# Kernel optimization log

Measured on AMD Instinct MI355X. Metric: run time of the kernel, lower is better.

Reference implementation:

```python
import jax, jax.numpy as jnp
import numpy as np

NUM_HEADS = 16
NUM_KV_HEADS = 4
HEAD_DIM = 128
ROPE_THETA = 10000.0
LN_EPS = 1e-5


def rotate_half(x):
    h = x.shape[-1] // 2
    return jnp.concatenate([-x[..., h:], x[..., :h]], axis=-1)


def setup_inputs() -> dict:
    key = jax.random.key(0)
    ks = jax.random.split(key, 12)
    B, S, H = 2, 2048, 2048
    qdim = NUM_HEADS * HEAD_DIM          # 2048
    kvdim = NUM_KV_HEADS * HEAD_DIM      # 512
    s = 1.0 / np.sqrt(H)
    return {
        'hidden_states': jax.random.normal(ks[0], (B, S, H), jnp.float32),
        'position_ids': jnp.arange(S, dtype=jnp.int32).reshape(1, S),
        'Wq': jax.random.normal(ks[1], (H, qdim), jnp.float32) * s,
        'Wk': jax.random.normal(ks[2], (H, kvdim), jnp.float32) * s,
        'Wv': jax.random.normal(ks[3], (H, kvdim), jnp.float32) * s,
        'Wo': jax.random.normal(ks[4], (qdim, H), jnp.float32) * (1.0 / np.sqrt(qdim)),
        'Wg1': jax.random.normal(ks[5], (H, NUM_HEADS), jnp.float32) * s,
        'bg1': jnp.zeros((NUM_HEADS,), jnp.float32),
        'Wg2': jax.random.normal(ks[6], (H, NUM_HEADS), jnp.float32) * s,
        'bg2': jnp.zeros((NUM_HEADS,), jnp.float32),
        'ln_gamma': jnp.ones((HEAD_DIM,), jnp.float32),
        'ln_beta': jnp.zeros((HEAD_DIM,), jnp.float32),
    }


def reference(hidden_states, position_ids, Wq, Wk, Wv, Wo, Wg1, bg1, Wg2, bg2, ln_gamma, ln_beta):
    B, S, H = hidden_states.shape
    dt = hidden_states.dtype

    # q/k/v projections -> (B, heads, S, head_dim)
    q = (hidden_states @ Wq).reshape(B, S, NUM_HEADS, HEAD_DIM).transpose(0, 2, 1, 3)
    k = (hidden_states @ Wk).reshape(B, S, NUM_KV_HEADS, HEAD_DIM).transpose(0, 2, 1, 3)
    v = (hidden_states @ Wv).reshape(B, S, NUM_KV_HEADS, HEAD_DIM).transpose(0, 2, 1, 3)

    # Llama RoPE
    inv_freq = 1.0 / (ROPE_THETA ** (jnp.arange(0, HEAD_DIM, 2, dtype=jnp.float32) / HEAD_DIM))
    freqs = position_ids.astype(jnp.float32)[..., None] * inv_freq  # (1, S, hd/2)
    emb = jnp.concatenate([freqs, freqs], axis=-1)                  # (1, S, hd)
    cos = jnp.cos(emb)[:, None].astype(dt)                          # (1, 1, S, hd)
    sin = jnp.sin(emb)[:, None].astype(dt)
    q = q * cos + rotate_half(q) * sin
    k = k * cos + rotate_half(k) * sin

    # GQA: repeat kv heads
    n_rep = NUM_HEADS // NUM_KV_HEADS
    k = jnp.repeat(k, n_rep, axis=1)
    v = jnp.repeat(v, n_rep, axis=1)

    # per-token per-head gates: (B, S, heads) -> (B, heads, S, 1)
    g1 = jax.nn.sigmoid(hidden_states @ Wg1 + bg1).transpose(0, 2, 1)[..., None]
    g2 = jax.nn.sigmoid(hidden_states @ Wg2 + bg2).transpose(0, 2, 1)[..., None]

    # value gating (weight_proj2)
    v = v * g2

    # causal softmax attention
    scores = jnp.einsum('bhqd,bhkd->bhqk', q, k) / np.sqrt(HEAD_DIM)
    causal = jnp.tril(jnp.ones((S, S), bool))
    scores = jnp.where(causal[None, None], scores, jnp.finfo(jnp.float32).min)
    probs = jax.nn.softmax(scores.astype(jnp.float32), axis=-1).astype(dt)
    o = jnp.einsum('bhqk,bhkd->bhqd', probs, v)  # (B, heads, S, hd)

    # per-head LayerNorm over head_dim, then output gating (weight_proj)
    mu = jnp.mean(o, axis=-1, keepdims=True)
    var = jnp.mean(jnp.square(o - mu), axis=-1, keepdims=True)
    o = (o - mu) / jnp.sqrt(var + LN_EPS) * ln_gamma + ln_beta
    o = o * g1

    o = o.transpose(0, 2, 1, 3).reshape(B, S, NUM_HEADS * HEAD_DIM)
    return o @ Wo
```

## Files before the change

### kernel.cpp

```cpp
#include <hip/hip_runtime.h>
#include <hip/hip_bf16.h>
#include <stdint.h>
#include <string.h>

using bf16 = __hip_bfloat16;
typedef __attribute__((ext_vector_type(8))) short bf16x8;
typedef __attribute__((ext_vector_type(4))) float f32x4;

#define DEV static __device__ __forceinline__

DEV bf16 tobf(float f) { return __float2bfloat16(f); }
DEV float tof(bf16 h) { return __bfloat162float(h); }

DEV void gload_lds16(const void* g, void* l) {
  __builtin_amdgcn_global_load_lds((__attribute__((address_space(1))) void*)g,
                                   (__attribute__((address_space(3))) void*)l,
                                   16, 0, 0);
}


__global__ void transpose_cast_k(const float* __restrict__ src, bf16* __restrict__ dst,
                                 int K, int N) {
  __shared__ float tile[32][33];
  int kb = blockIdx.x * 32, nb = blockIdx.y * 32;
  int tx = threadIdx.x, ty = threadIdx.y;
#pragma unroll
  for (int i = 0; i < 32; i += 8)
    tile[ty + i][tx] = src[(size_t)(kb + ty + i) * N + nb + tx];
  __syncthreads();
#pragma unroll
  for (int i = 0; i < 32; i += 8)
    dst[(size_t)(nb + ty + i) * K + kb + tx] = tobf(tile[tx][ty + i]);
}

__global__ void gw_transpose_k(const float* __restrict__ Wg1, const float* __restrict__ Wg2,
                               bf16* __restrict__ dstbase) {
  int g = blockIdx.x >> 4, r = blockIdx.x & 15;
  const float* src = g ? Wg2 : Wg1;
  bf16* dst = dstbase + (size_t)(3072 + g * 16 + r) * 2048;
  for (int k = threadIdx.x; k < 2048; k += 256) dst[k] = tobf(src[(size_t)k * 16 + r]);
}

__global__ void cast_x_k(const float* __restrict__ src, bf16* __restrict__ dst) {
  int i = blockIdx.x * blockDim.x + threadIdx.x;
  float4 v = ((const float4*)src)[i];
  bf16 t[4] = {tobf(v.x), tobf(v.y), tobf(v.z), tobf(v.w)};
  uint2 p; __builtin_memcpy(&p, t, 8);
  ((uint2*)dst)[i] = p;
}

__global__ void rope_table_k(const int* __restrict__ pos, float* __restrict__ cosT,
                             float* __restrict__ sinT) {
  int s = blockIdx.x, i = threadIdx.x;
  double inv = exp(-((double)(2 * i) / 128.0) * log(10000.0));
  float f = (float)pos[s] * (float)inv;
  cosT[s * 64 + i] = cosf(f);
  sinT[s * 64 + i] = sinf(f);
}

__global__ __launch_bounds__(256) void rope_apply_k(
    bf16* __restrict__ qkv, const float* __restrict__ cosT, const float* __restrict__ sinT) {
  int idx = blockIdx.x * 256 + threadIdx.x;
  int c = idx & 7, hh = idx >> 3;
  int head = hh % 20, t = hh / 20;
  int s = t & 2047;
  size_t base = (size_t)t * 3072 + (head < 16 ? head * 128 : 2048 + (head - 16) * 128);
  int d0 = c * 8;
  bf16x8 lo = *(const bf16x8*)(qkv + base + d0);
  bf16x8 hi = *(const bf16x8*)(qkv + base + d0 + 64);
  float4 c0 = *(const float4*)(cosT + s * 64 + d0);
  float4 c1 = *(const float4*)(cosT + s * 64 + d0 + 4);
  float4 s0 = *(const float4*)(sinT + s * 64 + d0);
  float4 s1 = *(const float4*)(sinT + s * 64 + d0 + 4);
  float cs[8] = {c0.x, c0.y, c0.z, c0.w, c1.x, c1.y, c1.z, c1.w};
  float sn[8] = {s0.x, s0.y, s0.z, s0.w, s1.x, s1.y, s1.z, s1.w};
  bf16x8 olo, ohi;
#pragma unroll
  for (int j = 0; j < 8; j++) {
    float a = tof(((const bf16*)&lo)[j]), b = tof(((const bf16*)&hi)[j]);
    ((bf16*)&olo)[j] = tobf(a * cs[j] - b * sn[j]);
    ((bf16*)&ohi)[j] = tobf(b * cs[j] + a * sn[j]);
  }
  *(bf16x8*)(qkv + base + d0) = olo;
  *(bf16x8*)(qkv + base + d0 + 64) = ohi;
}

__global__ __launch_bounds__(256, 2) void gemm_qkv_k(
    const bf16* __restrict__ A, const bf16* __restrict__ Bt, bf16* __restrict__ qkv,
    float* __restrict__ g1t, float* __restrict__ g2t,
    const float* __restrict__ bg1, const float* __restrict__ bg2) {
  constexpr int BK = 32, K = 2048;
  __shared__ bf16 sA[2][128 * BK];
  __shared__ bf16 sB[2][128 * BK];
  const int tid = threadIdx.x, wave = tid >> 6, lane = tid & 63;
  const int lhi = lane >> 4, llo = lane & 15;
  const int wm = wave >> 1, wn = wave & 1;
  const int bm = blockIdx.y, bn = blockIdx.x;
  const bf16* Ag = A + (size_t)bm * 128 * K;
  const bf16* Bg = Bt + (size_t)bn * 128 * K;

  f32x4 acc[4][4];
#pragma unroll
  for (int m = 0; m < 4; m++)
#pragma unroll
    for (int n = 0; n < 4; n++) acc[m][n] = f32x4{0.f, 0.f, 0.f, 0.f};

  auto stage = [&](int buf, int kt) {
#pragma unroll
    for (int i = 0; i < 2; i++) {
      int c = i * 256 + tid, row = c >> 2, c8 = c & 3;
      gload_lds16(Ag + (size_t)row * K + kt * BK + c8 * 8, &sA[buf][c * 8]);
    }
#pragma unroll
    for (int i = 0; i < 2; i++) {
      int c = i * 256 + tid, row = c >> 2, c8 = c & 3;
      gload_lds16(Bg + (size_t)row * K + kt * BK + c8 * 8, &sB[buf][c * 8]);
    }
  };

  const int NT = K / BK;
  stage(0, 0);
  for (int kt = 0; kt < NT; kt++) {
    __syncthreads();
    if (kt + 1 < NT) stage((kt + 1) & 1, kt + 1);
    const bf16* a_ = sA[kt & 1];
    const bf16* b_ = sB[kt & 1];
    bf16x8 af[4], bfr[4];
#pragma unroll
    for (int m = 0; m < 4; m++)
      af[m] = *(const bf16x8*)&a_[(wm * 64 + m * 16 + llo) * BK + lhi * 8];
#pragma unroll
    for (int n = 0; n < 4; n++)
      bfr[n] = *(const bf16x8*)&b_[(wn * 64 + n * 16 + llo) * BK + lhi * 8];
#pragma unroll
    for (int m = 0; m < 4; m++)
#pragma unroll
      for (int n = 0; n < 4; n++)
        acc[m][n] = __builtin_amdgcn_mfma_f32_16x16x32_bf16(af[m], bfr[n], acc[m][n], 0, 0, 0);
  }

  const int r0 = bm * 128 + wm * 64, c0 = bn * 128 + wn * 64;
#pragma unroll
  for (int m = 0; m < 4; m++)
#pragma unroll
    for (int n = 0; n < 4; n++) {
      int col = c0 + n * 16 + llo;
#pragma unroll
      for (int r = 0; r < 4; r++) {
        int row = r0 + m * 16 + lhi * 4 + r;
        if (col < 3072) {
          qkv[(size_t)row * 3072 + col] = tobf(acc[m][n][r]);
        } else if (col < 3104) {
          int idx = col - 3072, hh = idx & 15;
          float b = (idx < 16) ? bg1[hh] : bg2[hh];
          float v = 1.f / (1.f + __expf(-(acc[m][n][r] + b)));
          ((idx < 16) ? g1t : g2t)[(size_t)hh * 4096 + row] = v;
        }
      }
    }
}

__global__ __launch_bounds__(256, 2) void gemm_out_k(
    const bf16* __restrict__ A, const bf16* __restrict__ Bt, float* __restrict__ C,
    int M, int N, int K) {
  constexpr int BK = 32;
  __shared__ bf16 sA[2][128 * BK];
  __shared__ bf16 sB[2][128 * BK];
  const int tid = threadIdx.x, wave = tid >> 6, lane = tid & 63;
  const int lhi = lane >> 4, llo = lane & 15;
  const int wm = wave >> 1, wn = wave & 1;
  const int bm = blockIdx.y, bn = blockIdx.x;
  const bf16* Ag = A + (size_t)bm * 128 * K;
  const bf16* Bg = Bt + (size_t)bn * 128 * K;

  f32x4 acc[4][4];
#pragma unroll
  for (int m = 0; m < 4; m++)
#pragma unroll
    for (int n = 0; n < 4; n++) acc[m][n] = f32x4{0.f, 0.f, 0.f, 0.f};

  auto stage = [&](int buf, int kt) {
#pragma unroll
    for (int i = 0; i < 2; i++) {
      int c = i * 256 + tid, row = c >> 2, c8 = c & 3;
      gload_lds16(Ag + (size_t)row * K + kt * BK + c8 * 8, &sA[buf][c * 8]);
    }
#pragma unroll
    for (int i = 0; i < 2; i++) {
      int c = i * 256 + tid, row = c >> 2, c8 = c & 3;
      gload_lds16(Bg + (size_t)row * K + kt * BK + c8 * 8, &sB[buf][c * 8]);
    }
  };

  const int NT = K / BK;
  stage(0, 0);
  for (int kt = 0; kt < NT; kt++) {
    __syncthreads();
    if (kt + 1 < NT) stage((kt + 1) & 1, kt + 1);
    const bf16* a_ = sA[kt & 1];
    const bf16* b_ = sB[kt & 1];
    bf16x8 af[4], bfr[4];
#pragma unroll
    for (int m = 0; m < 4; m++)
      af[m] = *(const bf16x8*)&a_[(wm * 64 + m * 16 + llo) * BK + lhi * 8];
#pragma unroll
    for (int n = 0; n < 4; n++)
      bfr[n] = *(const bf16x8*)&b_[(wn * 64 + n * 16 + llo) * BK + lhi * 8];
#pragma unroll
    for (int m = 0; m < 4; m++)
#pragma unroll
      for (int n = 0; n < 4; n++)
        acc[m][n] = __builtin_amdgcn_mfma_f32_16x16x32_bf16(af[m], bfr[n], acc[m][n], 0, 0, 0);
  }

  const int r0 = bm * 128 + wm * 64, c0 = bn * 128 + wn * 64;
#pragma unroll
  for (int m = 0; m < 4; m++)
#pragma unroll
    for (int n = 0; n < 4; n++)
#pragma unroll
      for (int r = 0; r < 4; r++)
        C[(size_t)(r0 + m * 16 + lhi * 4 + r) * N + (c0 + n * 16 + llo)] = acc[m][n][r];
}

DEV void finalize_store(const f32x4 (&o)[8], int wave, int lhi, int llo, int tid,
                        int h, int qt, size_t tok0,
                        const float* __restrict__ g1t, const float* __restrict__ lng,
                        const float* __restrict__ lnb, bf16* sK, bf16* __restrict__ aout) {
  float sum[4] = {0, 0, 0, 0}, sq[4] = {0, 0, 0, 0};
#pragma unroll
  for (int dt = 0; dt < 8; dt++)
#pragma unroll
    for (int r = 0; r < 4; r++) {
      float v = o[dt][r];
      sum[r] += v;
      sq[r] += v * v;
    }
  float mu[4], rstd[4];
#pragma unroll
  for (int r = 0; r < 4; r++) {
    float s1 = sum[r], s2 = sq[r];
    s1 += __shfl_xor(s1, 1); s1 += __shfl_xor(s1, 2); s1 += __shfl_xor(s1, 4); s1 += __shfl_xor(s1, 8);
    s2 += __shfl_xor(s2, 1); s2 += __shfl_xor(s2, 2); s2 += __shfl_xor(s2, 4); s2 += __shfl_xor(s2, 8);
    float m_ = s1 * (1.f / 128.f);
    float var = s2 * (1.f / 128.f) - m_ * m_;
    mu[r] = m_;
    rstd[r] = rsqrtf(var + 1e-5f);
  }
  __syncthreads();
#pragma unroll
  for (int r = 0; r < 4; r++) {
    int lrow = wave * 16 + lhi * 4 + r;
    float gg = g1t[(size_t)h * 4096 + tok0 + qt * 64 + lrow];
#pragma unroll
    for (int dt = 0; dt < 8; dt++) {
      int d = dt * 16 + llo;
      float v = (o[dt][r] - mu[r]) * rstd[r] * lng[d] + lnb[d];
      sK[lrow * 128 + d] = tobf(v * gg);
    }
  }
  __syncthreads();
#pragma unroll
  for (int i = 0; i < 4; i++) {
    int c = i * 256 + tid, lr = c >> 4, c8 = c & 15;
    *(uint4*)(aout + (tok0 + qt * 64 + lr) * 2048 + h * 128 + c8 * 8) =
        *(const uint4*)&sK[lr * 128 + c8 * 8];
  }
}

__global__ __launch_bounds__(256, 2) void attn_split_k(
    const bf16* __restrict__ qkv, const float* __restrict__ g2t,
    const float* __restrict__ g1t, const float* __restrict__ lng,
    const float* __restrict__ lnb,
    float* __restrict__ pO, float* __restrict__ pML, bf16* __restrict__ aout) {
  constexpr int S = 2048, LD = 3072;
  const int bid = blockIdx.x;
  const int g = bid & 7, j = bid >> 3;
  const int hp = j & 1, u = j >> 1;
  int qt, k0, s;
  bool partial;
  if (u < 16) { qt = 16 + u; k0 = 0; s = 0; partial = true; }
  else {
    int p = (u - 16) >> 1;
    if (((u - 16) & 1) == 0) { qt = 15 - p; k0 = 0; s = 0; partial = false; }
    else { qt = 31 - p; k0 = 16; s = 1; partial = true; }
  }
  const int k1 = (u < 16) ? 16 : qt + 1;

  const int b = g >> 2, kvh = g & 3, h0 = kvh * 4 + hp * 2;
  const int tid = threadIdx.x, wave = tid >> 6, lane = tid & 63;
  const int lhi = lane >> 4, llo = lane & 15;
  const size_t tok0 = (size_t)b * S;

  __shared__ bf16 sK[64 * 128];
  __shared__ bf16 sV[128 * 64];
  __shared__ bf16 sP[4][2][16][72];

  const int qrow0 = qt * 64 + wave * 16;

  bf16x8 qf[2][4];
#pragma unroll
  for (int hh = 0; hh < 2; hh++) {
    const bf16* qg = qkv + (tok0 + qrow0 + llo) * LD + (h0 + hh) * 128;
#pragma unroll
    for (int dc = 0; dc < 4; dc++) qf[hh][dc] = *(const bf16x8*)(qg + dc * 32 + lhi * 8);
  }

  f32x4 oacc[2][8];
#pragma unroll
  for (int hh = 0; hh < 2; hh++)
#pragma unroll
    for (int i = 0; i < 8; i++) oacc[hh][i] = f32x4{0.f, 0.f, 0.f, 0.f};
  float mrow[2][4], lrow[2][4];
#pragma unroll
  for (int hh = 0; hh < 2; hh++)
#pragma unroll
    for (int r = 0; r < 4; r++) { mrow[hh][r] = -1e30f; lrow[hh][r] = 0.f; }
  const float scale = 0.08838834764831845f;

  uint4 kreg[4];
  bf16x8 vreg[4];
  float gvreg[2];
  const int vdg = tid >> 4;
  const int vkg = tid & 15;

  auto issue_loads = [&](int kt) {
#pragma unroll
    for (int i = 0; i < 4; i++) {
      int c = i * 256 + tid, row = c >> 4, c8 = c & 15;
      kreg[i] = *(const uint4*)(qkv + (tok0 + kt * 64 + row) * LD + 2048 + kvh * 128 + c8 * 8);
    }
#pragma unroll
    for (int r = 0; r < 4; r++)
      vreg[r] = *(const bf16x8*)(qkv + (tok0 + kt * 64 + vkg * 4 + r) * LD + 2560 +
                                 kvh * 128 + vdg * 8);
#pragma unroll
    for (int hh = 0; hh < 2; hh++)
      gvreg[hh] = g2t[(size_t)(h0 + hh) * 4096 + tok0 + kt * 64 + lane];
  };

  auto write_lds = [&]() {
#pragma unroll
    for (int i = 0; i < 4; i++) {
      int c = i * 256 + tid, row = c >> 4, c8 = c & 15;
      int eidx = (row * 128 + c8 * 8) ^ ((row & 7) << 3);
      *(uint4*)&sK[eidx] = kreg[i];
    }
#pragma unroll
    for (int e = 0; e < 8; e++) {
      int d = vdg * 8 + e;
      uint32_t lo = (uint32_t)(unsigned short)vreg[0][e] |
                    ((uint32_t)(unsigned short)vreg[1][e] << 16);
      uint32_t hi = (uint32_t)(unsigned short)vreg[2][e] |
                    ((uint32_t)(unsigned short)vreg[3][e] << 16);
      int eidx = (d * 64 + vkg * 4) ^ (e << 3);
      uint2 pk; pk.x = lo; pk.y = hi;
      *(uint2*)&sV[eidx] = pk;
    }
  };

  issue_loads(k0);
  for (int kt = k0; kt < k1; kt++) {
    __syncthreads();
    write_lds();
    float gv0 = gvreg[0], gv1 = gvreg[1];
    __syncthreads();
    if (kt + 1 < k1) issue_loads(kt + 1);

    const bool diag = (kt == qt);
#pragma unroll
    for (int hh = 0; hh < 2; hh++) {
      f32x4 sc[4];
#pragma unroll
      for (int ct = 0; ct < 4; ct++) {
        f32x4 acc = f32x4{0.f, 0.f, 0.f, 0.f};
#pragma unroll
        for (int dc = 0; dc < 4; dc++) {
          int row = ct * 16 + llo;
          bf16x8 kf = *(const bf16x8*)&sK[(row * 128 + dc * 32 + lhi * 8) ^ ((row & 7) << 3)];
          acc = __builtin_amdgcn_mfma_f32_16x16x32_bf16(qf[hh][dc], kf, acc, 0, 0, 0);
        }
        sc[ct] = acc;
      }
      float pm[4] = {-1e30f, -1e30f, -1e30f, -1e30f};
#pragma unroll
      for (int ct = 0; ct < 4; ct++) {
        int kv = kt * 64 + ct * 16 + llo;
#pragma unroll
        for (int r = 0; r < 4; r++) {
          float s_ = sc[ct][r] * scale;
          if (diag && kv > qrow0 + lhi * 4 + r) s_ = -1e30f;
          sc[ct][r] = s_;
          pm[r] = fmaxf(pm[r], s_);
        }
      }
#pragma unroll
      for (int r = 0; r < 4; r++) {
        float v = pm[r];
        v = fmaxf(v, __shfl_xor(v, 1));
        v = fmaxf(v, __shfl_xor(v, 2));
        v = fmaxf(v, __shfl_xor(v, 4));
        v = fmaxf(v, __shfl_xor(v, 8));
        pm[r] = v;
      }
      int need = 0;
#pragma unroll
      for (int r = 0; r < 4; r++) need |= (pm[r] > mrow[hh][r]) ? 1 : 0;
      if (__any(need)) {
#pragma unroll
        for (int r = 0; r < 4; r++) {
          float mnew = fmaxf(mrow[hh][r], pm[r]);
          float al = __expf(mrow[hh][r] - mnew);
          mrow[hh][r] = mnew;
          lrow[hh][r] *= al;
#pragma unroll
          for (int i = 0; i < 8; i++) oacc[hh][i][r] *= al;
        }
      }
      float gv = hh ? gv1 : gv0;
      float g2v[4];
#pragma unroll
      for (int ct = 0; ct < 4; ct++) g2v[ct] = __shfl(gv, ct * 16 + llo);
      float rs[4] = {0.f, 0.f, 0.f, 0.f};
#pragma unroll
      for (int ct = 0; ct < 4; ct++) {
#pragma unroll
        for (int r = 0; r < 4; r++) {
          float p = __expf(sc[ct][r] - mrow[hh][r]);
          rs[r] += p;
          sP[wave][hh][lhi * 4 + r][ct * 16 + llo] = tobf(p * g2v[ct]);
        }
      }
#pragma unroll
      for (int r = 0; r < 4; r++) {
        float v = rs[r];
        v += __shfl_xor(v, 1); v += __shfl_xor(v, 2); v += __shfl_xor(v, 4); v += __shfl_xor(v, 8);
        lrow[hh][r] += v;
      }
    }
#pragma unroll
    for (int kc = 0; kc < 2; kc++) {
      bf16x8 pf0 = *(const bf16x8*)&sP[wave][0][llo][kc * 32 + lhi * 8];
      bf16x8 pf1 = *(const bf16x8*)&sP[wave][1][llo][kc * 32 + lhi * 8];
#pragma unroll
      for (int dt = 0; dt < 8; dt++) {
        int d = dt * 16 + llo;
        bf16x8 vf = *(const bf16x8*)&sV[(d * 64 + kc * 32 + lhi * 8) ^ ((d & 7) << 3)];
        oacc[0][dt] = __builtin_amdgcn_mfma_f32_16x16x32_bf16(pf0, vf, oacc[0][dt], 0, 0, 0);
        oacc[1][dt] = __builtin_amdgcn_mfma_f32_16x16x32_bf16(pf1, vf, oacc[1][dt], 0, 0, 0);
      }
    }
  }

  if (partial) {
    const int combo = (qt - 16) * 2 + s;
#pragma unroll
    for (int hh = 0; hh < 2; hh++) {
      const int sub = (g * 2 + hp) * 2 + hh;
      f32x4* dst = (f32x4*)pO + (size_t)(combo * 32 + sub) * 2048;
#pragma unroll
      for (int dt = 0; dt < 8; dt++)
        dst[(wave * 8 + dt) * 64 + lane] = oacc[hh][dt];
      if (llo == 0) {
#pragma unroll
        for (int r = 0; r < 4; r++) {
          int row = wave * 16 + lhi * 4 + r;
          float* pm = pML + ((size_t)(combo * 32 + sub) * 64 + row) * 2;
          pm[0] = mrow[hh][r];
          pm[1] = lrow[hh][r];
        }
      }
    }
  } else {
#pragma unroll
    for (int hh = 0; hh < 2; hh++) {
      float inv[4];
#pragma unroll
      for (int r = 0; r < 4; r++) inv[r] = 1.f / lrow[hh][r];
      f32x4 o[8];
#pragma unroll
      for (int dt = 0; dt < 8; dt++)
#pragma unroll
        for (int r = 0; r < 4; r++) o[dt][r] = oacc[hh][dt][r] * inv[r];
      finalize_store(o, wave, lhi, llo, tid, h0 + hh, qt, tok0, g1t, lng, lnb, sK, aout);
    }
  }
}

__global__ __launch_bounds__(256) void attn_combine_k(
    const float* __restrict__ pO, const float* __restrict__ pML,
    const float* __restrict__ g1t, const float* __restrict__ lng,
    const float* __restrict__ lnb, bf16* __restrict__ aout) {
  __shared__ bf16 sK[64 * 128];
  const int bid = blockIdx.x;
  const int g = bid & 7, j = bid >> 3;
  const int hp = j & 1, qt16 = j >> 1;
  const int qt = 16 + qt16;
  const int b = g >> 2, kvh = g & 3, h0 = kvh * 4 + hp * 2;
  const int tid = threadIdx.x, wave = tid >> 6, lane = tid & 63;
  const int lhi = lane >> 4, llo = lane & 15;
  const size_t tok0 = (size_t)b * 2048;
  const int c0 = qt16 * 2, c1 = qt16 * 2 + 1;
#pragma unroll
  for (int hh = 0; hh < 2; hh++) {
    const int sub = (g * 2 + hp) * 2 + hh;
    const f32x4* p0 = (const f32x4*)pO + (size_t)(c0 * 32 + sub) * 2048;
    const f32x4* p1 = (const f32x4*)pO + (size_t)(c1 * 32 + sub) * 2048;
    float w0[4], w1[4], inv[4];
#pragma unroll
    for (int r = 0; r < 4; r++) {
      int row = wave * 16 + lhi * 4 + r;
      const float* q0 = pML + ((size_t)(c0 * 32 + sub) * 64 + row) * 2;
      const float* q1 = pML + ((size_t)(c1 * 32 + sub) * 64 + row) * 2;
      float m0 = q0[0], l0 = q0[1], m1 = q1[0], l1 = q1[1];
      float ms = fmaxf(m0, m1);
      w0[r] = __expf(m0 - ms);
      w1[r] = __expf(m1 - ms);
      inv[r] = 1.f / (w0[r] * l0 + w1[r] * l1);
    }
    f32x4 o[8];
#pragma unroll
    for (int dt = 0; dt < 8; dt++) {
      f32x4 a = p0[(wave * 8 + dt) * 64 + lane];
      f32x4 c = p1[(wave * 8 + dt) * 64 + lane];
#pragma unroll
      for (int r = 0; r < 4; r++) o[dt][r] = (w0[r] * a[r] + w1[r] * c[r]) * inv[r];
    }
    finalize_store(o, wave, lhi, llo, tid, h0 + hh, qt, tok0, g1t, lng, lnb, sK, aout);
  }
}

extern "C" void kernel_launch(void* const* d_in, const int* in_sizes, int n_in,
                              void* d_out, int out_size, void* d_ws, size_t ws_size,
                              hipStream_t stream) {
  (void)in_sizes; (void)n_in; (void)out_size; (void)ws_size;
  const float* X   = (const float*)d_in[0];
  const int*   pos = (const int*)d_in[1];
  const float* Wq  = (const float*)d_in[2];
  const float* Wk  = (const float*)d_in[3];
  const float* Wv  = (const float*)d_in[4];
  const float* Wo  = (const float*)d_in[5];
  const float* Wg1 = (const float*)d_in[6];
  const float* bg1 = (const float*)d_in[7];
  const float* Wg2 = (const float*)d_in[8];
  const float* bg2 = (const float*)d_in[9];
  const float* lng = (const float*)d_in[10];
  const float* lnb = (const float*)d_in[11];

  char* ws = (char*)d_ws;
  size_t off = 0;
  auto alloc = [&](size_t bytes) {
    void* p = ws + off;
    off += (bytes + 255) & ~(size_t)255;
    return p;
  };
  bf16*  WT   = (bf16*)alloc(3200ull * 2048 * 2);
  bf16*  WoT  = (bf16*)alloc(2048ull * 2048 * 2);
  bf16*  Xbf  = (bf16*)alloc(4096ull * 2048 * 2);
  bf16*  qkv  = (bf16*)alloc(4096ull * 3072 * 2);
  bf16*  attn = (bf16*)alloc(4096ull * 2048 * 2);
  float* cosT = (float*)alloc(2048ull * 64 * 4);
  float* sinT = (float*)alloc(2048ull * 64 * 4);
  float* g1t  = (float*)alloc(16ull * 4096 * 4);
  float* g2t  = (float*)alloc(16ull * 4096 * 4);
  float* pO   = (float*)alloc(32ull * 32 * 8192 * 4);
  float* pML  = (float*)alloc(32ull * 32 * 64 * 2 * 4);

  dim3 tb(32, 8);
  transpose_cast_k<<<dim3(64, 64), tb, 0, stream>>>(Wq, WT, 2048, 2048);
  transpose_cast_k<<<dim3(64, 16), tb, 0, stream>>>(Wk, WT + 2048ull * 2048, 2048, 512);
  transpose_cast_k<<<dim3(64, 16), tb, 0, stream>>>(Wv, WT + 2560ull * 2048, 2048, 512);
  transpose_cast_k<<<dim3(64, 64), tb, 0, stream>>>(Wo, WoT, 2048, 2048);
  gw_transpose_k<<<32, 256, 0, stream>>>(Wg1, Wg2, WT);
  cast_x_k<<<8192, 256, 0, stream>>>(X, Xbf);
  rope_table_k<<<2048, 64, 0, stream>>>(pos, cosT, sinT);

  gemm_qkv_k<<<dim3(25, 32), 256, 0, stream>>>(Xbf, WT, qkv, g1t, g2t, bg1, bg2);
  rope_apply_k<<<2560, 256, 0, stream>>>(qkv, cosT, sinT);
  attn_split_k<<<768, 256, 0, stream>>>(qkv, g2t, g1t, lng, lnb, pO, pML, attn);
  attn_combine_k<<<256, 256, 0, stream>>>(pO, pML, g1t, lng, lnb, attn);
  gemm_out_k<<<dim3(16, 32), 256, 0, stream>>>(attn, WoT, (float*)d_out, 4096, 2048, 2048);
}
```

Before: 296.4 us.

## Split causal attention into 8-tile KV chunks with table-driven scheduling

Replaces the two-way split of causal attention with chunks of at most 8 KV tiles, so query tiles beyond 8 are split into 2-4 partials. A lookup table orders the work units longest-first for load balancing, and the combine kernel now merges up to 4 partials. Launch bounds rise to 3 blocks per SM, and the next tile's loads are issued before the barrier. The aim is better balance and occupancy, at the cost of more partial-result traffic, more combine work and possible register pressure.

```diff
diff --git a/kernel.cpp b/kernel.cpp
--- a/kernel.cpp
+++ b/kernel.cpp
@@ -268,7 +268,28 @@
   }
 }
 
-__global__ __launch_bounds__(256, 2) void attn_split_k(
+DEV int pid_base(int qt) {
+  return qt < 8 ? qt : qt < 16 ? 2 * qt - 8 : qt < 24 ? 3 * qt - 24 : 4 * qt - 48;
+}
+
+__device__ const unsigned char UNIT_TAB[80] = {
+  124,125,126,127,
+  120,121,122, 116,117,118, 112,113,114,
+  108,109,110, 104,105,106, 100,101,102,
+   96, 97, 98,  92, 93, 94,
+   88, 89,  84, 85,  80, 81,  76, 77,
+   72, 73,  68, 69,  64, 65,  60, 61,
+   56, 52, 48, 44, 40, 36, 32, 28,
+  123, 90, 57, 24,
+  119, 86, 53, 20,
+  115, 82, 49, 16,
+  111, 78, 45, 12,
+  107, 74, 41,  8,
+  103, 70, 37,  4,
+   99, 66, 33,  0
+};
+
+__global__ __launch_bounds__(256, 3) void attn_split_k(
     const bf16* __restrict__ qkv, const float* __restrict__ g2t,
     const float* __restrict__ g1t, const float* __restrict__ lng,
     const float* __restrict__ lnb,
@@ -277,15 +298,10 @@
   const int bid = blockIdx.x;
   const int g = bid & 7, j = bid >> 3;
   const int hp = j & 1, u = j >> 1;
-  int qt, k0, s;
-  bool partial;
-  if (u < 16) { qt = 16 + u; k0 = 0; s = 0; partial = true; }
-  else {
-    int p = (u - 16) >> 1;
-    if (((u - 16) & 1) == 0) { qt = 15 - p; k0 = 0; s = 0; partial = false; }
-    else { qt = 31 - p; k0 = 16; s = 1; partial = true; }
-  }
-  const int k1 = (u < 16) ? 16 : qt + 1;
+  const int e = UNIT_TAB[u];
+  const int qt = e >> 2, s = e & 3;
+  const int k0 = s * 8, k1 = min(s * 8 + 8, qt + 1);
+  const bool partial = (qt >= 8);
 
   const int b = g >> 2, kvh = g & 3, h0 = kvh * 4 + hp * 2;
   const int tid = threadIdx.x, wave = tid >> 6, lane = tid & 63;
@@ -347,13 +363,13 @@
       *(uint4*)&sK[eidx] = kreg[i];
     }
 #pragma unroll
-    for (int e = 0; e < 8; e++) {
-      int d = vdg * 8 + e;
-      uint32_t lo = (uint32_t)(unsigned short)vreg[0][e] |
-                    ((uint32_t)(unsigned short)vreg[1][e] << 16);
-      uint32_t hi = (uint32_t)(unsigned short)vreg[2][e] |
-                    ((uint32_t)(unsigned short)vreg[3][e] << 16);
-      int eidx = (d * 64 + vkg * 4) ^ (e << 3);
+    for (int e2 = 0; e2 < 8; e2++) {
+      int d = vdg * 8 + e2;
+      uint32_t lo = (uint32_t)(unsigned short)vreg[0][e2] |
+                    ((uint32_t)(unsigned short)vreg[1][e2] << 16);
+      uint32_t hi = (uint32_t)(unsigned short)vreg[2][e2] |
+                    ((uint32_t)(unsigned short)vreg[3][e2] << 16);
+      int eidx = (d * 64 + vkg * 4) ^ (e2 << 3);
       uint2 pk; pk.x = lo; pk.y = hi;
       *(uint2*)&sV[eidx] = pk;
     }
@@ -364,8 +380,8 @@
     __syncthreads();
     write_lds();
     float gv0 = gvreg[0], gv1 = gvreg[1];
+    if (kt + 1 < k1) issue_loads(kt + 1);
     __syncthreads();
-    if (kt + 1 < k1) issue_loads(kt + 1);
 
     const bool diag = (kt == qt);
 #pragma unroll
@@ -453,11 +469,11 @@
   }
 
   if (partial) {
-    const int combo = (qt - 16) * 2 + s;
+    const int pid = pid_base(qt) + s;
 #pragma unroll
     for (int hh = 0; hh < 2; hh++) {
       const int sub = (g * 2 + hp) * 2 + hh;
-      f32x4* dst = (f32x4*)pO + (size_t)(combo * 32 + sub) * 2048;
+      f32x4* dst = (f32x4*)pO + (size_t)(pid * 32 + sub) * 2048;
 #pragma unroll
       for (int dt = 0; dt < 8; dt++)
         dst[(wave * 8 + dt) * 64 + lane] = oacc[hh][dt];
@@ -465,7 +481,7 @@
 #pragma unroll
         for (int r = 0; r < 4; r++) {
           int row = wave * 16 + lhi * 4 + r;
-          float* pm = pML + ((size_t)(combo * 32 + sub) * 64 + row) * 2;
+          float* pm = pML + ((size_t)(pid * 32 + sub) * 64 + row) * 2;
           pm[0] = mrow[hh][r];
           pm[1] = lrow[hh][r];
         }
@@ -494,37 +510,49 @@
   __shared__ bf16 sK[64 * 128];
   const int bid = blockIdx.x;
   const int g = bid & 7, j = bid >> 3;
-  const int hp = j & 1, qt16 = j >> 1;
-  const int qt = 16 + qt16;
+  const int hp = j & 1, qtc = j >> 1;
+  const int qt = 8 + qtc;
+  const int ns = (qt < 16) ? 2 : (qt < 24) ? 3 : 4;
+  const int p0id = pid_base(qt);
   const int b = g >> 2, kvh = g & 3, h0 = kvh * 4 + hp * 2;
   const int tid = threadIdx.x, wave = tid >> 6, lane = tid & 63;
   const int lhi = lane >> 4, llo = lane & 15;
   const size_t tok0 = (size_t)b * 2048;
-  const int c0 = qt16 * 2, c1 = qt16 * 2 + 1;
 #pragma unroll
   for (int hh = 0; hh < 2; hh++) {
     const int sub = (g * 2 + hp) * 2 + hh;
-    const f32x4* p0 = (const f32x4*)pO + (size_t)(c0 * 32 + sub) * 2048;
-    const f32x4* p1 = (const f32x4*)pO + (size_t)(c1 * 32 + sub) * 2048;
-    float w0[4], w1[4], inv[4];
+    float w[4][4], inv[4];
 #pragma unroll
     for (int r = 0; r < 4; r++) {
       int row = wave * 16 + lhi * 4 + r;
-      const float* q0 = pML + ((size_t)(c0 * 32 + sub) * 64 + row) * 2;
-      const float* q1 = pML + ((size_t)(c1 * 32 + sub) * 64 + row) * 2;
-      float m0 = q0[0], l0 = q0[1], m1 = q1[0], l1 = q1[1];
-      float ms = fmaxf(m0, m1);
-      w0[r] = __expf(m0 - ms);
-      w1[r] = __expf(m1 - ms);
-      inv[r] = 1.f / (w0[r] * l0 + w1[r] * l1);
+      float m[4], l[4], ms = -1e30f;
+#pragma unroll
+      for (int sp = 0; sp < 4; sp++)
+        if (sp < ns) {
+          const float* q = pML + ((size_t)((p0id + sp) * 32 + sub) * 64 + row) * 2;
+          m[sp] = q[0]; l[sp] = q[1];
+          ms = fmaxf(ms, m[sp]);
+        }
+      float L = 0.f;
+#pragma unroll
+      for (int sp = 0; sp < 4; sp++)
+        if (sp < ns) { w[sp][r] = __expf(m[sp] - ms); L += w[sp][r] * l[sp]; }
+      inv[r] = 1.f / L;
     }
     f32x4 o[8];
 #pragma unroll
     for (int dt = 0; dt < 8; dt++) {
-      f32x4 a = p0[(wave * 8 + dt) * 64 + lane];
-      f32x4 c = p1[(wave * 8 + dt) * 64 + lane];
-#pragma unroll
-      for (int r = 0; r < 4; r++) o[dt][r] = (w0[r] * a[r] + w1[r] * c[r]) * inv[r];
+      f32x4 a = f32x4{0.f, 0.f, 0.f, 0.f};
+#pragma unroll
+      for (int sp = 0; sp < 4; sp++)
+        if (sp < ns) {
+          f32x4 c = ((const f32x4*)pO + (size_t)((p0id + sp) * 32 + sub) * 2048)
+                        [(wave * 8 + dt) * 64 + lane];
+#pragma unroll
+          for (int r = 0; r < 4; r++) a[r] += w[sp][r] * c[r];
+        }
+#pragma unroll
+      for (int r = 0; r < 4; r++) o[dt][r] = a[r] * inv[r];
     }
     finalize_store(o, wave, lhi, llo, tid, h0 + hh, qt, tok0, g1t, lng, lnb, sK, aout);
   }
@@ -563,8 +591,8 @@
   float* sinT = (float*)alloc(2048ull * 64 * 4);
   float* g1t  = (float*)alloc(16ull * 4096 * 4);
   float* g2t  = (float*)alloc(16ull * 4096 * 4);
-  float* pO   = (float*)alloc(32ull * 32 * 8192 * 4);
-  float* pML  = (float*)alloc(32ull * 32 * 64 * 2 * 4);
+  float* pO   = (float*)alloc(80ull * 32 * 8192 * 4);
+  float* pML  = (float*)alloc(80ull * 32 * 64 * 2 * 4);
 
   dim3 tb(32, 8);
   transpose_cast_k<<<dim3(64, 64), tb, 0, stream>>>(Wq, WT, 2048, 2048);
@@ -577,7 +605,7 @@
 
   gemm_qkv_k<<<dim3(25, 32), 256, 0, stream>>>(Xbf, WT, qkv, g1t, g2t, bg1, bg2);
   rope_apply_k<<<2560, 256, 0, stream>>>(qkv, cosT, sinT);
-  attn_split_k<<<768, 256, 0, stream>>>(qkv, g2t, g1t, lng, lnb, pO, pML, attn);
-  attn_combine_k<<<256, 256, 0, stream>>>(pO, pML, g1t, lng, lnb, attn);
+  attn_split_k<<<1280, 256, 0, stream>>>(qkv, g2t, g1t, lng, lnb, pO, pML, attn);
+  attn_combine_k<<<384, 256, 0, stream>>>(pO, pML, g1t, lng, lnb, attn);
   gemm_out_k<<<dim3(16, 32), 256, 0, stream>>>(attn, WoT, (float*)d_out, 4096, 2048, 2048);
 }
```

Result: slower. 570.2 us (+92.4%).
